# Kernel optimization log

Hardware: AMD Instinct MI355X
Metric: run time of the kernel (lower is better)

Reference implementation:

```python
import jax, jax.numpy as jnp
import numpy as np

N, E, B = 100000, 1600000, 1024
EPS = 1e-5


def setup_inputs() -> dict:
    key = jax.random.key(0)
    ks = jax.random.split(key, 32)
    w = lambda k, shape: (jax.random.normal(k, shape, jnp.float32) * 0.05)
    inp = {
        'x': jax.random.normal(ks[0], (N, 20), jnp.float32),
        'edge_index': jax.random.randint(ks[1], (2, E), 0, N, dtype=jnp.int32),
        'batch': jnp.sort(jax.random.randint(ks[2], (N,), 0, B, dtype=jnp.int32)),
        # GCN layer 1 (20->64) + BN
        'W1': w(ks[3], (20, 64)), 'b1': jnp.zeros(64), 'g1': jnp.ones(64), 'bt1': jnp.zeros(64),
        # GCN layer 2 (64->64) + BN
        'W2': w(ks[4], (64, 64)), 'b2': jnp.zeros(64), 'g2': jnp.ones(64), 'bt2': jnp.zeros(64),
        # GCN layer 3 (64->128)
        'W3': w(ks[5], (64, 128)), 'b3': jnp.zeros(128),
        # operation head
        'Wo1': w(ks[6], (128, 64)), 'bo1': jnp.zeros(64), 'Wo2': w(ks[7], (64, 13)), 'bo2': jnp.zeros(13),
        # param head
        'Wp1': w(ks[8], (128, 64)), 'bp1': jnp.zeros(64), 'Wp2': w(ks[9], (64, 64)), 'bp2': jnp.zeros(64), 'Wp3': w(ks[10], (64, 1)), 'bp3': jnp.zeros(1),
        # done head
        'Wd1': w(ks[11], (128, 64)), 'bd1': jnp.zeros(64), 'Wd2': w(ks[12], (64, 2)), 'bd2': jnp.zeros(2),
    }
    return inp


def _gcn(x, W, b, src, dst):
    # PyG GCNConv: sym-normalized A+I, linear first, bias after aggregation
    h = x @ W  # [N, F]
    deg = jax.ops.segment_sum(jnp.ones_like(src, jnp.float32), dst, N) + 1.0  # +1 self loop
    dinv = jax.lax.rsqrt(deg)
    norm = dinv[src] * dinv[dst]  # [E]
    agg = jax.ops.segment_sum(h[src] * norm[:, None], dst, N)
    agg = agg + h * (dinv * dinv)[:, None]  # self-loop term
    return agg + b


def _bn(x, g, bt):
    mu = jnp.mean(x, axis=0)
    var = jnp.mean((x - mu) ** 2, axis=0)  # biased var (torch BN training math)
    return (x - mu) * jax.lax.rsqrt(var + EPS) * g + bt


def reference(x, edge_index, batch, W1, b1, g1, bt1, W2, b2, g2, bt2, W3, b3,
              Wo1, bo1, Wo2, bo2, Wp1, bp1, Wp2, bp2, Wp3, bp3, Wd1, bd1, Wd2, bd2):
    src, dst = edge_index[0], edge_index[1]
    h = jax.nn.relu(_bn(_gcn(x, W1, b1, src, dst), g1, bt1))  # dropout = identity (eval)
    h = jax.nn.relu(_bn(_gcn(h, W2, b2, src, dst), g2, bt2))
    h = _gcn(h, W3, b3, src, dst)  # [N, 128]
    # global mean pool over graphs
    sums = jax.ops.segment_sum(h, batch, B)
    cnt = jax.ops.segment_sum(jnp.ones((N,), jnp.float32), batch, B)
    enc = sums / jnp.maximum(cnt, 1.0)[:, None]  # [B, 128]
    op_logits = jax.nn.relu(enc @ Wo1 + bo1) @ Wo2 + bo2  # [B, 13]
    p = jax.nn.relu(enc @ Wp1 + bp1)
    p = jax.nn.relu(p @ Wp2 + bp2)
    param_value = p @ Wp3 + bp3  # [B, 1]
    done_logits = jax.nn.relu(enc @ Wd1 + bd1) @ Wd2 + bd2  # [B, 2]
    return op_logits, param_value, done_logits, enc
```

## Files before the change

kernel.cpp:

```cpp
#include <hip/hip_runtime.h>

#define BN_EPS 1e-5f

constexpr int BSH = 9;
constexpr int MAXB = 200;
constexpr int CAP = 12288;
constexpr int BINCAP = 32;
constexpr int FLUSH = 16;
constexpr int SBLK = 256;

typedef unsigned short u16;
typedef unsigned int u32;

__device__ __forceinline__ float b2f(u16 h) {
  return __uint_as_float(((u32)h) << 16);
}
__device__ __forceinline__ u16 f2b(float f) {
  u32 u = __float_as_uint(f);
  return (u16)((u + 0x7FFFu + ((u >> 16) & 1u)) >> 16);
}


__global__ void initk(int* __restrict__ gcur, float* __restrict__ bn, int NB) {
  int t = blockIdx.x * blockDim.x + threadIdx.x;
  if (t < NB) gcur[t] = t * CAP;
  if (t < 512) bn[t] = 0.f;
}

__global__ void bound_kernel(const int* __restrict__ batch, int* __restrict__ goffs, int N, int B) {
  int i = blockIdx.x * blockDim.x + threadIdx.x;
  if (i < N) {
    int b = batch[i];
    int p = (i == 0) ? -1 : batch[i - 1];
    for (int g = p + 1; g <= b; ++g) goffs[g] = i;
    if (i == N - 1) {
      for (int g = b + 1; g <= B; ++g) goffs[g] = N;
    }
  }
}


__global__ __launch_bounds__(256) void passA(const int* __restrict__ dst, const int* __restrict__ src,
                                             int* __restrict__ gcur, unsigned long long* __restrict__ temp,
                                             int E, int NB) {
  __shared__ unsigned long long bins[MAXB * BINCAP];
  __shared__ int bcnt[MAXB];
  int tid = threadIdx.x;
  for (int b = tid; b < NB; b += 256) bcnt[b] = 0;
  __syncthreads();
  int chunk = (E + gridDim.x - 1) / gridDim.x;
  int e0 = blockIdx.x * chunk;
  int e1 = min(e0 + chunk, E);
  for (int base = e0; base < e1; base += 1024) {
#pragma unroll
    for (int j = 0; j < 4; ++j) {
      int e = base + tid * 4 + j;
      if (e < e1) {
        int d = dst[e];
        int s = src[e];
        int b = d >> BSH;
        unsigned long long pk = ((unsigned long long)(unsigned)s << 32) | (unsigned)d;
        int slot = atomicAdd(&bcnt[b], 1);
        if (slot < BINCAP) {
          bins[b * BINCAP + slot] = pk;
        } else {
          int p = atomicAdd(&gcur[b], 1);
          temp[p] = pk;
        }
      }
    }
    __syncthreads();
    if (tid < NB) {
      int c = min(bcnt[tid], BINCAP);
      while (c >= FLUSH) {
        int p = atomicAdd(&gcur[tid], FLUSH);
        for (int j = 0; j < FLUSH; ++j) temp[p + j] = bins[tid * BINCAP + j];
        c -= FLUSH;
        for (int j = 0; j < c; ++j) bins[tid * BINCAP + j] = bins[tid * BINCAP + FLUSH + j];
      }
      bcnt[tid] = c;
    }
    __syncthreads();
  }
  if (tid < NB) {
    int c = min(bcnt[tid], BINCAP);
    if (c > 0) {
      int p = atomicAdd(&gcur[tid], c);
      for (int j = 0; j < c; ++j) temp[p + j] = bins[tid * BINCAP + j];
    }
  }
}

__global__ __launch_bounds__(512) void passB1(const unsigned long long* __restrict__ temp,
                                              const int* __restrict__ gcur,
                                              int* __restrict__ deg, float* __restrict__ dinv, int N) {
  __shared__ int h[512];
  int b = blockIdx.x, t = threadIdx.x;
  h[t] = 0;
  __syncthreads();
  int cnt = min(gcur[b] - b * CAP, CAP);
  const unsigned long long* tp = temp + (size_t)b * CAP;
  for (int i = t; i < cnt; i += 512) {
    int d = (int)(tp[i] & 0xffffffffu);
    atomicAdd(&h[d & 511], 1);
  }
  __syncthreads();
  int node = (b << BSH) + t;
  if (node < N) {
    deg[node] = h[t];
    dinv[node] = rsqrtf((float)h[t] + 1.f);
  }
}

__global__ __launch_bounds__(512) void passB2(const unsigned long long* __restrict__ temp,
                                              const int* __restrict__ gcur,
                                              const int* __restrict__ offs,
                                              int* __restrict__ csr, int N) {
  __shared__ int lofs[512];
  __shared__ int lcnt[512];
  int b = blockIdx.x, t = threadIdx.x;
  int node = (b << BSH) + t;
  lofs[t] = offs[min(node, N)];
  lcnt[t] = 0;
  __syncthreads();
  int cnt = min(gcur[b] - b * CAP, CAP);
  const unsigned long long* tp = temp + (size_t)b * CAP;
  for (int i = t; i < cnt; i += 512) {
    unsigned long long pk = tp[i];
    int d = (int)(pk & 0xffffffffu) & 511;
    int s = (int)(pk >> 32);
    int pos = lofs[d] + atomicAdd(&lcnt[d], 1);
    csr[pos] = s;
  }
}


__global__ __launch_bounds__(1024) void scan_p1(const int* __restrict__ cnt,
                                                int* __restrict__ offs,
                                                int* __restrict__ bsum, int n) {
  __shared__ int sh[1024];
  int t = threadIdx.x;
  int i = blockIdx.x * 1024 + t;
  int v = (i < n) ? cnt[i] : 0;
  sh[t] = v;
  __syncthreads();
  for (int d = 1; d < 1024; d <<= 1) {
    int x = (t >= d) ? sh[t - d] : 0;
    __syncthreads();
    sh[t] += x;
    __syncthreads();
  }
  if (i < n) offs[i] = sh[t] - v;
  if (t == 1023) bsum[blockIdx.x] = sh[t];
}

__global__ void scan_p2(int* __restrict__ bsum, int nb) {
  __shared__ int sh[128];
  int t = threadIdx.x;
  int v = (t < nb) ? bsum[t] : 0;
  sh[t] = v;
  __syncthreads();
  for (int d = 1; d < 128; d <<= 1) {
    int x = (t >= d) ? sh[t - d] : 0;
    __syncthreads();
    sh[t] += x;
    __syncthreads();
  }
  if (t < nb) bsum[t] = sh[t] - v;
}

__global__ __launch_bounds__(1024) void scan_p3(int* __restrict__ offs,
                                                const int* __restrict__ bsum, int n, int E) {
  int i = blockIdx.x * 1024 + threadIdx.x;
  if (i < n) offs[i] += bsum[blockIdx.x];
  if (i == 0) offs[n] = E;
}


__global__ void prex_kernel(const float* __restrict__ x, const float* __restrict__ dinv,
                            u16* __restrict__ x16, int N) {
  int stride = gridDim.x * blockDim.x;
  for (int i = blockIdx.x * blockDim.x + threadIdx.x; i < N * 32; i += stride) {
    int row = i >> 5, f = i & 31;
    float v = (f < 20) ? x[row * 20 + f] * dinv[row] : 0.f;
    x16[i] = f2b(v);
  }
}


__global__ __launch_bounds__(256) void agg32x_kernel(const u16* __restrict__ x16,
                                                     const int* __restrict__ offs,
                                                     const int* __restrict__ csr,
                                                     float* __restrict__ out, int n) {
  int lane = threadIdx.x & 63;
  int wid = threadIdx.x >> 6;
  int half = lane >> 5, f = lane & 31;
  int gw = blockIdx.x * 4 + wid, nw = gridDim.x * 4;
  for (int i = gw; i < n; i += nw) {
    float acc = half ? 0.f : b2f(x16[(size_t)i * 32 + f]);
    int st = offs[i], en = offs[i + 1];
    for (int base = st; base < en; base += 64) {
      int idx = base + lane;
      int v = (idx < en) ? csr[idx] : 0;
      int cnt = min(64, en - base);
      int j = 0;
      for (; j + 3 < cnt; j += 4) {
        int s0 = __shfl(v, j + half);
        int s1 = __shfl(v, j + 2 + half);
        acc += b2f(x16[(size_t)s0 * 32 + f]) + b2f(x16[(size_t)s1 * 32 + f]);
      }
      for (; j < cnt; ++j) {
        int s = __shfl(v, j);
        if (!half) acc += b2f(x16[(size_t)s * 32 + f]);
      }
    }
    acc += __shfl_xor(acc, 32);
    if (!half) out[(size_t)i * 32 + f] = acc;
  }
}

template <bool SCALE>
__global__ __launch_bounds__(256) void agg64t_kernel(const u16* __restrict__ z16,
                                                     const float* __restrict__ tav,
                                                     const float* __restrict__ tcv,
                                                     const int* __restrict__ offs,
                                                     const int* __restrict__ csr,
                                                     const float* __restrict__ dinv,
                                                     float* __restrict__ out, int n) {
  int lane = threadIdx.x & 63;
  int wid = threadIdx.x >> 6;
  float ta = tav[lane], tc = tcv[lane];
  int gw = blockIdx.x * 4 + wid, nw = gridDim.x * 4;
  for (int i = gw; i < n; i += nw) {
    float di = dinv[i];
    float acc = fmaxf(b2f(z16[(size_t)i * 64 + lane]) * ta + tc, 0.f) * di;
    int st = offs[i], en = offs[i + 1];
    for (int base = st; base < en; base += 64) {
      int idx = base + lane;
      int v = (idx < en) ? csr[idx] : 0;
      int cnt = min(64, en - base);
      int j = 0;
      for (; j + 3 < cnt; j += 4) {
        int s0 = __shfl(v, j), s1 = __shfl(v, j + 1);
        int s2 = __shfl(v, j + 2), s3 = __shfl(v, j + 3);
        float d0 = dinv[s0], d1 = dinv[s1], d2 = dinv[s2], d3 = dinv[s3];
        acc += fmaxf(b2f(z16[(size_t)s0 * 64 + lane]) * ta + tc, 0.f) * d0 +
               fmaxf(b2f(z16[(size_t)s1 * 64 + lane]) * ta + tc, 0.f) * d1 +
               fmaxf(b2f(z16[(size_t)s2 * 64 + lane]) * ta + tc, 0.f) * d2 +
               fmaxf(b2f(z16[(size_t)s3 * 64 + lane]) * ta + tc, 0.f) * d3;
      }
      for (; j < cnt; ++j) {
        int s = __shfl(v, j);
        acc += fmaxf(b2f(z16[(size_t)s * 64 + lane]) * ta + tc, 0.f) * dinv[s];
      }
    }
    if (SCALE) acc *= di;
    out[(size_t)i * 64 + lane] = acc;
  }
}


template <int K, int AS>
__global__ __launch_bounds__(256) void gemm_agg(const float* __restrict__ A, const float* __restrict__ W,
                                                const float* __restrict__ bias, const float* __restrict__ dinv,
                                                u16* __restrict__ z16, int n) {
  __shared__ float Ws[K * 64];
  __shared__ float As[128 * (K + 1)];
  int tid = threadIdx.x;
  int row0 = blockIdx.x * 128;
  for (int i = tid; i < K * 64; i += 256) Ws[i] = W[i];
  for (int i = tid; i < 128 * K; i += 256) {
    int r = i / K, k = i - r * K;
    int gr = row0 + r;
    As[r * (K + 1) + k] = (gr < n) ? A[(size_t)gr * AS + k] : 0.f;
  }
  __syncthreads();
  int rg = tid >> 2;
  int fs = tid & 3;
  float acc0[16], acc1[16];
#pragma unroll
  for (int j = 0; j < 16; ++j) { acc0[j] = 0.f; acc1[j] = 0.f; }
  const float* a0 = &As[(2 * rg) * (K + 1)];
  const float* a1 = &As[(2 * rg + 1) * (K + 1)];
  const float* wb = &Ws[fs * 16];
  for (int k = 0; k < K; ++k) {
    float x0 = a0[k], x1 = a1[k];
#pragma unroll
    for (int j = 0; j < 16; ++j) {
      float w = wb[k * 64 + j];
      acc0[j] += x0 * w;
      acc1[j] += x1 * w;
    }
  }
  int base = fs * 16;
  int r0 = row0 + 2 * rg;
  if (r0 < n) {
    float dv = dinv[r0];
    u32 pk[8];
#pragma unroll
    for (int j = 0; j < 8; ++j) {
      float o0 = acc0[2 * j] * dv + bias[base + 2 * j];
      float o1 = acc0[2 * j + 1] * dv + bias[base + 2 * j + 1];
      pk[j] = (u32)f2b(o0) | ((u32)f2b(o1) << 16);
    }
    uint4* zp = (uint4*)&z16[(size_t)r0 * 64 + base];
    zp[0] = make_uint4(pk[0], pk[1], pk[2], pk[3]);
    zp[1] = make_uint4(pk[4], pk[5], pk[6], pk[7]);
  }
  int r1 = r0 + 1;
  if (r1 < n) {
    float dv = dinv[r1];
    u32 pk[8];
#pragma unroll
    for (int j = 0; j < 8; ++j) {
      float o0 = acc1[2 * j] * dv + bias[base + 2 * j];
      float o1 = acc1[2 * j + 1] * dv + bias[base + 2 * j + 1];
      pk[j] = (u32)f2b(o0) | ((u32)f2b(o1) << 16);
    }
    uint4* zp = (uint4*)&z16[(size_t)r1 * 64 + base];
    zp[0] = make_uint4(pk[0], pk[1], pk[2], pk[3]);
    zp[1] = make_uint4(pk[4], pk[5], pk[6], pk[7]);
  }
}


__global__ __launch_bounds__(256) void bn_stats(const u16* __restrict__ z16,
                                                float* __restrict__ partial, int N) {
  int lane = threadIdx.x & 63, wid = threadIdx.x >> 6;
  int gw = blockIdx.x * 4 + wid, nw = gridDim.x * 4;
  float s = 0.f, q = 0.f;
  for (int r = gw; r < N; r += nw) {
    float v = b2f(z16[(size_t)r * 64 + lane]);
    s += v;
    q += v * v;
  }
  __shared__ float sh[2][4][64];
  sh[0][wid][lane] = s;
  sh[1][wid][lane] = q;
  __syncthreads();
  if (wid == 0) {
    float ts = sh[0][0][lane] + sh[0][1][lane] + sh[0][2][lane] + sh[0][3][lane];
    float tq = sh[1][0][lane] + sh[1][1][lane] + sh[1][2][lane] + sh[1][3][lane];
    partial[blockIdx.x * 128 + lane] = ts;
    partial[blockIdx.x * 128 + 64 + lane] = tq;
  }
}

__global__ __launch_bounds__(1024) void bn_final_kernel(const float* __restrict__ partial,
                                                        const float* __restrict__ g,
                                                        const float* __restrict__ bt,
                                                        float* __restrict__ a, float* __restrict__ c,
                                                        float n) {
  __shared__ float sh[16][128];
  int t = threadIdx.x;
  int grp = t >> 6, lane = t & 63;
  float s = 0.f, q = 0.f;
#pragma unroll
  for (int k = 0; k < 16; ++k) {
    int i = grp * 16 + k;
    s += partial[i * 128 + lane];
    q += partial[i * 128 + 64 + lane];
  }
  sh[grp][lane] = s;
  sh[grp][64 + lane] = q;
  __syncthreads();
  for (int str = 8; str >= 1; str >>= 1) {
    if (grp < str) {
      sh[grp][lane] += sh[grp + str][lane];
      sh[grp][64 + lane] += sh[grp + str][64 + lane];
    }
    __syncthreads();
  }
  if (grp == 0) {
    float mu = sh[0][lane] / n;
    float var = fmaxf(sh[0][64 + lane] / n - mu * mu, 0.f);
    float rstd = rsqrtf(var + BN_EPS);
    float av = g[lane] * rstd;
    a[lane] = av;
    c[lane] = bt[lane] - mu * av;
  }
}


__global__ __launch_bounds__(64) void pool_kernel(const float* __restrict__ v3,
                                                  const int* __restrict__ goffs,
                                                  float* __restrict__ ep, int B) {
  int b = blockIdx.x, t = threadIdx.x;
  int st = goffs[b], en = goffs[b + 1];
  float s = 0.f;
  int r = st;
  for (; r + 1 < en; r += 2) s += v3[(size_t)r * 64 + t] + v3[(size_t)(r + 1) * 64 + t];
  if (r < en) s += v3[(size_t)r * 64 + t];
  int c = en - st;
  ep[(size_t)b * 64 + t] = s / (float)max(c, 1);
}


__global__ __launch_bounds__(256) void heads_kernel(
    const float* __restrict__ ep, const int* __restrict__ goffs,
    const float* __restrict__ W3, const float* __restrict__ b3,
    const float* __restrict__ Wo1, const float* __restrict__ bo1,
    const float* __restrict__ Wo2, const float* __restrict__ bo2,
    const float* __restrict__ Wp1, const float* __restrict__ bp1,
    const float* __restrict__ Wp2, const float* __restrict__ bp2,
    const float* __restrict__ Wp3, const float* __restrict__ bp3,
    const float* __restrict__ Wd1, const float* __restrict__ bd1,
    const float* __restrict__ Wd2, const float* __restrict__ bd2,
    float* __restrict__ out_op, float* __restrict__ out_p, float* __restrict__ out_d,
    float* __restrict__ enc_out, int B) {
  __shared__ float epl[16 * 64];
  __shared__ float es[16 * 128];
  __shared__ float t1[16 * 64];
  __shared__ float t2[16 * 64];
  int tid = threadIdx.x;
  int g0 = blockIdx.x * 16;
  for (int i = tid; i < 16 * 64; i += 256) epl[i] = ep[(size_t)g0 * 64 + i];
  __syncthreads();
  for (int o = tid; o < 16 * 128; o += 256) {
    int r = o >> 7, c = o & 127;
    float a = b3[c];
    for (int k = 0; k < 64; ++k) a += epl[r * 64 + k] * W3[k * 128 + c];
    if (goffs[g0 + r + 1] - goffs[g0 + r] == 0) a = 0.f;
    es[o] = a;
    enc_out[(size_t)(g0 + r) * 128 + c] = a;
  }
  __syncthreads();
  for (int o = tid; o < 16 * 64; o += 256) {
    int r = o >> 6, c = o & 63;
    float a = bo1[c];
    for (int k = 0; k < 128; k++) a += es[r * 128 + k] * Wo1[k * 64 + c];
    t1[o] = fmaxf(a, 0.f);
  }
  __syncthreads();
  for (int o = tid; o < 16 * 13; o += 256) {
    int r = o / 13, c = o - r * 13;
    float a = bo2[c];
    for (int k = 0; k < 64; k++) a += t1[r * 64 + k] * Wo2[k * 13 + c];
    out_op[(size_t)(g0 + r) * 13 + c] = a;
  }
  __syncthreads();
  for (int o = tid; o < 16 * 64; o += 256) {
    int r = o >> 6, c = o & 63;
    float a = bp1[c];
    for (int k = 0; k < 128; k++) a += es[r * 128 + k] * Wp1[k * 64 + c];
    t1[o] = fmaxf(a, 0.f);
  }
  __syncthreads();
  for (int o = tid; o < 16 * 64; o += 256) {
    int r = o >> 6, c = o & 63;
    float a = bp2[c];
    for (int k = 0; k < 64; k++) a += t1[r * 64 + k] * Wp2[k * 64 + c];
    t2[o] = fmaxf(a, 0.f);
  }
  __syncthreads();
  for (int o = tid; o < 16; o += 256) {
    float a = bp3[0];
    for (int k = 0; k < 64; k++) a += t2[o * 64 + k] * Wp3[k];
    out_p[g0 + o] = a;
  }
  __syncthreads();
  for (int o = tid; o < 16 * 64; o += 256) {
    int r = o >> 6, c = o & 63;
    float a = bd1[c];
    for (int k = 0; k < 128; k++) a += es[r * 128 + k] * Wd1[k * 64 + c];
    t1[o] = fmaxf(a, 0.f);
  }
  __syncthreads();
  for (int o = tid; o < 16 * 2; o += 256) {
    int r = o >> 1, c = o & 1;
    float a = bd2[c];
    for (int k = 0; k < 64; k++) a += t1[r * 64 + k] * Wd2[k * 2 + c];
    out_d[(size_t)(g0 + r) * 2 + c] = a;
  }
}


extern "C" void kernel_launch(void* const* d_in, const int* in_sizes, int n_in,
                              void* d_out, int out_size, void* d_ws, size_t ws_size,
                              hipStream_t stream) {
  const float* x   = (const float*)d_in[0];
  const int*   ei  = (const int*)d_in[1];
  const int*   bat = (const int*)d_in[2];
  const float* W1 = (const float*)d_in[3];  const float* b1  = (const float*)d_in[4];
  const float* g1 = (const float*)d_in[5];  const float* bt1 = (const float*)d_in[6];
  const float* W2 = (const float*)d_in[7];  const float* b2  = (const float*)d_in[8];
  const float* g2 = (const float*)d_in[9];  const float* bt2 = (const float*)d_in[10];
  const float* W3 = (const float*)d_in[11]; const float* b3  = (const float*)d_in[12];
  const float* Wo1 = (const float*)d_in[13]; const float* bo1 = (const float*)d_in[14];
  const float* Wo2 = (const float*)d_in[15]; const float* bo2 = (const float*)d_in[16];
  const float* Wp1 = (const float*)d_in[17]; const float* bp1 = (const float*)d_in[18];
  const float* Wp2 = (const float*)d_in[19]; const float* bp2 = (const float*)d_in[20];
  const float* Wp3 = (const float*)d_in[21]; const float* bp3 = (const float*)d_in[22];
  const float* Wd1 = (const float*)d_in[23]; const float* bd1 = (const float*)d_in[24];
  const float* Wd2 = (const float*)d_in[25]; const float* bd2 = (const float*)d_in[26];

  int N = in_sizes[0] / 20;
  int E = in_sizes[1] / 2;
  int B = out_size / 144;
  const int* esrc = ei;
  const int* edst = ei + E;
  int NB = (N + (1 << BSH) - 1) >> BSH;

  char* ws = (char*)d_ws;
  size_t off = 0;
  auto alloc = [&](size_t bytes) -> char* {
    char* p = ws + off;
    off = (off + bytes + 255) & ~(size_t)255;
    return p;
  };
  int*   gcur  = (int*)alloc((size_t)NB * 4);
  int*   deg   = (int*)alloc((size_t)N * 4);
  float* dinv  = (float*)alloc((size_t)N * 4);
  int*   offs  = (int*)alloc(((size_t)N + 1) * 4);
  int*   bsum  = (int*)alloc(128 * 4);
  int*   goffs = (int*)alloc(((size_t)B + 1) * 4);
  float* bn    = (float*)alloc(512 * 4);
  float* partial = (float*)alloc((size_t)SBLK * 128 * 4);
  unsigned long long* temp = (unsigned long long*)alloc((size_t)NB * CAP * 8);
  int*   csr   = (int*)alloc((size_t)E * 4);
  u16*   x16   = (u16*)alloc((size_t)N * 32 * 2);
  u16*   z16   = (u16*)alloc((size_t)N * 64 * 2);
  float* aggf  = (float*)alloc((size_t)N * 64 * 4);
  float* ep    = (float*)alloc((size_t)B * 64 * 4);

  float* ta1 = bn + 256, *tc1 = bn + 320;
  float* ta2 = bn + 384, *tc2 = bn + 448;

  float* out_op = (float*)d_out;
  float* out_p  = out_op + (size_t)B * 13;
  float* out_d  = out_p + B;
  float* enc    = out_d + (size_t)B * 2;

  hipLaunchKernelGGL(initk, dim3(2), dim3(256), 0, stream, gcur, bn, NB);
  hipLaunchKernelGGL(bound_kernel, dim3((N + 255) / 256), dim3(256), 0, stream, bat, goffs, N, B);
  hipLaunchKernelGGL(passA, dim3(256), dim3(256), 0, stream, edst, esrc, gcur, temp, E, NB);
  hipLaunchKernelGGL(passB1, dim3(NB), dim3(512), 0, stream, temp, gcur, deg, dinv, N);
  int nb1 = (N + 1023) / 1024;
  hipLaunchKernelGGL(scan_p1, dim3(nb1), dim3(1024), 0, stream, deg, offs, bsum, N);
  hipLaunchKernelGGL(scan_p2, dim3(1), dim3(128), 0, stream, bsum, nb1);
  hipLaunchKernelGGL(scan_p3, dim3(nb1), dim3(1024), 0, stream, offs, bsum, N, E);
  hipLaunchKernelGGL(passB2, dim3(NB), dim3(512), 0, stream, temp, gcur, offs, csr, N);

  int gblocks = (N + 127) / 128;
  hipLaunchKernelGGL(prex_kernel, dim3(2048), dim3(256), 0, stream, x, dinv, x16, N);
  hipLaunchKernelGGL(agg32x_kernel, dim3(2048), dim3(256), 0, stream, x16, offs, csr, aggf, N);
  hipLaunchKernelGGL((gemm_agg<20, 32>), dim3(gblocks), dim3(256), 0, stream,
                     aggf, W1, b1, dinv, z16, N);
  hipLaunchKernelGGL(bn_stats, dim3(SBLK), dim3(256), 0, stream, z16, partial, N);
  hipLaunchKernelGGL(bn_final_kernel, dim3(1), dim3(1024), 0, stream,
                     partial, g1, bt1, ta1, tc1, (float)N);
  hipLaunchKernelGGL((agg64t_kernel<false>), dim3(2048), dim3(256), 0, stream,
                     z16, ta1, tc1, offs, csr, dinv, aggf, N);
  hipLaunchKernelGGL((gemm_agg<64, 64>), dim3(gblocks), dim3(256), 0, stream,
                     aggf, W2, b2, dinv, z16, N);
  hipLaunchKernelGGL(bn_stats, dim3(SBLK), dim3(256), 0, stream, z16, partial, N);
  hipLaunchKernelGGL(bn_final_kernel, dim3(1), dim3(1024), 0, stream,
                     partial, g2, bt2, ta2, tc2, (float)N);
  hipLaunchKernelGGL((agg64t_kernel<true>), dim3(2048), dim3(256), 0, stream,
                     z16, ta2, tc2, offs, csr, dinv, aggf, N);
  hipLaunchKernelGGL(pool_kernel, dim3(B), dim3(64), 0, stream, aggf, goffs, ep, B);
  hipLaunchKernelGGL(heads_kernel, dim3(B / 16), dim3(256), 0, stream, ep, goffs, W3, b3,
                     Wo1, bo1, Wo2, bo2, Wp1, bp1, Wp2, bp2, Wp3, bp3, Wd1, bd1, Wd2, bd2,
                     out_op, out_p, out_d, enc, B);
}
```

Before: 496.6 us.

## Fuse BN statistics into GEMM epilogue, merge init kernel, scalarize gather indices

Batch-norm sum and sum-of-squares are now reduced inside the gemm_agg epilogue through wave shuffles and shared memory, with per-block partials written out. This removes the separate bn_stats pass that re-read z16, and bn_final now loops over a variable block count. The init kernel is folded into bound_kernel, and the aggregation loop uses readfirstlane to make neighbor indices scalar and splits the sum into two accumulators for more ILP. One side effect is that statistics are now taken from fp32 values rather than the rounded bf16 ones, and bn_final has more partials to reduce.

```diff
diff --git a/kernel.cpp b/kernel.cpp
--- a/kernel.cpp
+++ b/kernel.cpp
@@ -7,7 +7,6 @@
 constexpr int CAP = 12288;
 constexpr int BINCAP = 32;
 constexpr int FLUSH = 16;
-constexpr int SBLK = 256;
 
 typedef unsigned short u16;
 typedef unsigned int u32;
@@ -21,14 +20,10 @@
 }
 
 
-__global__ void initk(int* __restrict__ gcur, float* __restrict__ bn, int NB) {
-  int t = blockIdx.x * blockDim.x + threadIdx.x;
-  if (t < NB) gcur[t] = t * CAP;
-  if (t < 512) bn[t] = 0.f;
-}
-
-__global__ void bound_kernel(const int* __restrict__ batch, int* __restrict__ goffs, int N, int B) {
+__global__ void bound_kernel(const int* __restrict__ batch, int* __restrict__ goffs,
+                             int* __restrict__ gcur, int N, int B, int NB) {
   int i = blockIdx.x * blockDim.x + threadIdx.x;
+  if (i < NB) gcur[i] = i * CAP;
   if (i < N) {
     int b = batch[i];
     int p = (i == 0) ? -1 : batch[i - 1];
@@ -234,6 +229,7 @@
   for (int i = gw; i < n; i += nw) {
     float di = dinv[i];
     float acc = fmaxf(b2f(z16[(size_t)i * 64 + lane]) * ta + tc, 0.f) * di;
+    float acc2 = 0.f;
     int st = offs[i], en = offs[i + 1];
     for (int base = st; base < en; base += 64) {
       int idx = base + lane;
@@ -241,19 +237,23 @@
       int cnt = min(64, en - base);
       int j = 0;
       for (; j + 3 < cnt; j += 4) {
-        int s0 = __shfl(v, j), s1 = __shfl(v, j + 1);
-        int s2 = __shfl(v, j + 2), s3 = __shfl(v, j + 3);
-        float d0 = dinv[s0], d1 = dinv[s1], d2 = dinv[s2], d3 = dinv[s3];
-        acc += fmaxf(b2f(z16[(size_t)s0 * 64 + lane]) * ta + tc, 0.f) * d0 +
-               fmaxf(b2f(z16[(size_t)s1 * 64 + lane]) * ta + tc, 0.f) * d1 +
-               fmaxf(b2f(z16[(size_t)s2 * 64 + lane]) * ta + tc, 0.f) * d2 +
-               fmaxf(b2f(z16[(size_t)s3 * 64 + lane]) * ta + tc, 0.f) * d3;
+        int s0 = __builtin_amdgcn_readfirstlane(__shfl(v, j));
+        int s1 = __builtin_amdgcn_readfirstlane(__shfl(v, j + 1));
+        int s2 = __builtin_amdgcn_readfirstlane(__shfl(v, j + 2));
+        int s3 = __builtin_amdgcn_readfirstlane(__shfl(v, j + 3));
+        float z0 = b2f(z16[(size_t)s0 * 64 + lane]);
+        float z1 = b2f(z16[(size_t)s1 * 64 + lane]);
+        float z2 = b2f(z16[(size_t)s2 * 64 + lane]);
+        float z3 = b2f(z16[(size_t)s3 * 64 + lane]);
+        acc  += fmaxf(z0 * ta + tc, 0.f) * dinv[s0] + fmaxf(z1 * ta + tc, 0.f) * dinv[s1];
+        acc2 += fmaxf(z2 * ta + tc, 0.f) * dinv[s2] + fmaxf(z3 * ta + tc, 0.f) * dinv[s3];
       }
       for (; j < cnt; ++j) {
-        int s = __shfl(v, j);
+        int s = __builtin_amdgcn_readfirstlane(__shfl(v, j));
         acc += fmaxf(b2f(z16[(size_t)s * 64 + lane]) * ta + tc, 0.f) * dinv[s];
       }
     }
+    acc += acc2;
     if (SCALE) acc *= di;
     out[(size_t)i * 64 + lane] = acc;
   }
@@ -263,9 +263,10 @@
 template <int K, int AS>
 __global__ __launch_bounds__(256) void gemm_agg(const float* __restrict__ A, const float* __restrict__ W,
                                                 const float* __restrict__ bias, const float* __restrict__ dinv,
-                                                u16* __restrict__ z16, int n) {
+                                                u16* __restrict__ z16, float* __restrict__ partial, int n) {
   __shared__ float Ws[K * 64];
   __shared__ float As[128 * (K + 1)];
+  __shared__ float red[4][4][32];
   int tid = threadIdx.x;
   int row0 = blockIdx.x * 128;
   for (int i = tid; i < K * 64; i += 256) Ws[i] = W[i];
@@ -294,59 +295,68 @@
   }
   int base = fs * 16;
   int r0 = row0 + 2 * rg;
+  int r1 = r0 + 1;
+  float dv0 = (r0 < n) ? dinv[r0] : 0.f;
+  float dv1 = (r1 < n) ? dinv[r1] : 0.f;
+  u32 pk0[8], pk1[8];
+  u32 w0 = 0, w1 = 0;
+#pragma unroll
+  for (int j = 0; j < 16; ++j) {
+    float t0 = acc0[j] * dv0 + bias[base + j];
+    float t1 = acc1[j] * dv1 + bias[base + j];
+    if (r0 >= n) t0 = 0.f;
+    if (r1 >= n) t1 = 0.f;
+    if ((j & 1) == 0) {
+      w0 = f2b(t0);
+      w1 = f2b(t1);
+    } else {
+      pk0[j >> 1] = w0 | ((u32)f2b(t0) << 16);
+      pk1[j >> 1] = w1 | ((u32)f2b(t1) << 16);
+    }
+    acc0[j] = t0 + t1;
+    acc1[j] = t0 * t0 + t1 * t1;
+  }
   if (r0 < n) {
-    float dv = dinv[r0];
-    u32 pk[8];
+    uint4* zp = (uint4*)&z16[(size_t)r0 * 64 + base];
+    zp[0] = make_uint4(pk0[0], pk0[1], pk0[2], pk0[3]);
+    zp[1] = make_uint4(pk0[4], pk0[5], pk0[6], pk0[7]);
+  }
+  if (r1 < n) {
+    uint4* zp = (uint4*)&z16[(size_t)r1 * 64 + base];
+    zp[0] = make_uint4(pk1[0], pk1[1], pk1[2], pk1[3]);
+    zp[1] = make_uint4(pk1[4], pk1[5], pk1[6], pk1[7]);
+  }
 #pragma unroll
-    for (int j = 0; j < 8; ++j) {
-      float o0 = acc0[2 * j] * dv + bias[base + 2 * j];
-      float o1 = acc0[2 * j + 1] * dv + bias[base + 2 * j + 1];
-      pk[j] = (u32)f2b(o0) | ((u32)f2b(o1) << 16);
-    }
-    uint4* zp = (uint4*)&z16[(size_t)r0 * 64 + base];
-    zp[0] = make_uint4(pk[0], pk[1], pk[2], pk[3]);
-    zp[1] = make_uint4(pk[4], pk[5], pk[6], pk[7]);
-  }
-  int r1 = r0 + 1;
-  if (r1 < n) {
-    float dv = dinv[r1];
-    u32 pk[8];
+  for (int j = 0; j < 16; ++j) {
+    acc0[j] += __shfl_xor(acc0[j], 4);
+    acc1[j] += __shfl_xor(acc1[j], 4);
+    acc0[j] += __shfl_xor(acc0[j], 8);
+    acc1[j] += __shfl_xor(acc1[j], 8);
+    acc0[j] += __shfl_xor(acc0[j], 16);
+    acc1[j] += __shfl_xor(acc1[j], 16);
+    acc0[j] += __shfl_xor(acc0[j], 32);
+    acc1[j] += __shfl_xor(acc1[j], 32);
+  }
+  int lane = tid & 63, wid = tid >> 6;
+  if (lane < 4) {
 #pragma unroll
-    for (int j = 0; j < 8; ++j) {
-      float o0 = acc1[2 * j] * dv + bias[base + 2 * j];
-      float o1 = acc1[2 * j + 1] * dv + bias[base + 2 * j + 1];
-      pk[j] = (u32)f2b(o0) | ((u32)f2b(o1) << 16);
-    }
-    uint4* zp = (uint4*)&z16[(size_t)r1 * 64 + base];
-    zp[0] = make_uint4(pk[0], pk[1], pk[2], pk[3]);
-    zp[1] = make_uint4(pk[4], pk[5], pk[6], pk[7]);
-  }
-}
-
-
-__global__ __launch_bounds__(256) void bn_stats(const u16* __restrict__ z16,
-                                                float* __restrict__ partial, int N) {
-  int lane = threadIdx.x & 63, wid = threadIdx.x >> 6;
-  int gw = blockIdx.x * 4 + wid, nw = gridDim.x * 4;
-  float s = 0.f, q = 0.f;
-  for (int r = gw; r < N; r += nw) {
-    float v = b2f(z16[(size_t)r * 64 + lane]);
-    s += v;
-    q += v * v;
-  }
-  __shared__ float sh[2][4][64];
-  sh[0][wid][lane] = s;
-  sh[1][wid][lane] = q;
-  __syncthreads();
-  if (wid == 0) {
-    float ts = sh[0][0][lane] + sh[0][1][lane] + sh[0][2][lane] + sh[0][3][lane];
-    float tq = sh[1][0][lane] + sh[1][1][lane] + sh[1][2][lane] + sh[1][3][lane];
-    partial[blockIdx.x * 128 + lane] = ts;
-    partial[blockIdx.x * 128 + 64 + lane] = tq;
-  }
-}
-
-__global__ __launch_bounds__(1024) void bn_final_kernel(const float* __restrict__ partial,
+    for (int j = 0; j < 16; ++j) {
+      red[wid][lane][j] = acc0[j];
+      red[wid][lane][16 + j] = acc1[j];
+    }
+  }
+  __syncthreads();
+  if (tid < 128) {
+    int f = tid & 63;
+    int half = tid >> 6;
+    int fsi = f >> 4, fj = (f & 15) + (half ? 16 : 0);
+    float v = red[0][fsi][fj] + red[1][fsi][fj] + red[2][fsi][fj] + red[3][fsi][fj];
+    partial[(size_t)blockIdx.x * 128 + half * 64 + f] = v;
+  }
+}
+
+
+__global__ __launch_bounds__(1024) void bn_final_kernel(const float* __restrict__ partial, int nb,
                                                         const float* __restrict__ g,
                                                         const float* __restrict__ bt,
                                                         float* __restrict__ a, float* __restrict__ c,
@@ -355,11 +365,9 @@
   int t = threadIdx.x;
   int grp = t >> 6, lane = t & 63;
   float s = 0.f, q = 0.f;
-#pragma unroll
-  for (int k = 0; k < 16; ++k) {
-    int i = grp * 16 + k;
-    s += partial[i * 128 + lane];
-    q += partial[i * 128 + 64 + lane];
+  for (int i = grp; i < nb; i += 16) {
+    s += partial[(size_t)i * 128 + lane];
+    q += partial[(size_t)i * 128 + 64 + lane];
   }
   sh[grp][lane] = s;
   sh[grp][64 + lane] = q;
@@ -515,7 +523,7 @@
   int*   bsum  = (int*)alloc(128 * 4);
   int*   goffs = (int*)alloc(((size_t)B + 1) * 4);
   float* bn    = (float*)alloc(512 * 4);
-  float* partial = (float*)alloc((size_t)SBLK * 128 * 4);
+  float* partial = (float*)alloc((size_t)1024 * 128 * 4);
   unsigned long long* temp = (unsigned long long*)alloc((size_t)NB * CAP * 8);
   int*   csr   = (int*)alloc((size_t)E * 4);
   u16*   x16   = (u16*)alloc((size_t)N * 32 * 2);
@@ -531,8 +539,8 @@
   float* out_d  = out_p + B;
   float* enc    = out_d + (size_t)B * 2;
 
-  hipLaunchKernelGGL(initk, dim3(2), dim3(256), 0, stream, gcur, bn, NB);
-  hipLaunchKernelGGL(bound_kernel, dim3((N + 255) / 256), dim3(256), 0, stream, bat, goffs, N, B);
+  hipLaunchKernelGGL(bound_kernel, dim3((N + 255) / 256), dim3(256), 0, stream,
+                     bat, goffs, gcur, N, B, NB);
   hipLaunchKernelGGL(passA, dim3(256), dim3(256), 0, stream, edst, esrc, gcur, temp, E, NB);
   hipLaunchKernelGGL(passB1, dim3(NB), dim3(512), 0, stream, temp, gcur, deg, dinv, N);
   int nb1 = (N + 1023) / 1024;
@@ -545,17 +553,15 @@
   hipLaunchKernelGGL(prex_kernel, dim3(2048), dim3(256), 0, stream, x, dinv, x16, N);
   hipLaunchKernelGGL(agg32x_kernel, dim3(2048), dim3(256), 0, stream, x16, offs, csr, aggf, N);
   hipLaunchKernelGGL((gemm_agg<20, 32>), dim3(gblocks), dim3(256), 0, stream,
-                     aggf, W1, b1, dinv, z16, N);
-  hipLaunchKernelGGL(bn_stats, dim3(SBLK), dim3(256), 0, stream, z16, partial, N);
+                     aggf, W1, b1, dinv, z16, partial, N);
   hipLaunchKernelGGL(bn_final_kernel, dim3(1), dim3(1024), 0, stream,
-                     partial, g1, bt1, ta1, tc1, (float)N);
+                     partial, gblocks, g1, bt1, ta1, tc1, (float)N);
   hipLaunchKernelGGL((agg64t_kernel<false>), dim3(2048), dim3(256), 0, stream,
                      z16, ta1, tc1, offs, csr, dinv, aggf, N);
   hipLaunchKernelGGL((gemm_agg<64, 64>), dim3(gblocks), dim3(256), 0, stream,
-                     aggf, W2, b2, dinv, z16, N);
-  hipLaunchKernelGGL(bn_stats, dim3(SBLK), dim3(256), 0, stream, z16, partial, N);
+                     aggf, W2, b2, dinv, z16, partial, N);
   hipLaunchKernelGGL(bn_final_kernel, dim3(1), dim3(1024), 0, stream,
-                     partial, g2, bt2, ta2, tc2, (float)N);
+                     partial, gblocks, g2, bt2, ta2, tc2, (float)N);
   hipLaunchKernelGGL((agg64t_kernel<true>), dim3(2048), dim3(256), 0, stream,
                      z16, ta2, tc2, offs, csr, dinv, aggf, N);
   hipLaunchKernelGGL(pool_kernel, dim3(B), dim3(64), 0, stream, aggf, goffs, ep, B);
```

Result: faster. 479.6 us (-3.4%).
